# Kernel optimization log

Hardware: AMD Instinct MI355X
Metric: run time of the kernel (lower is better)

Reference implementation:

```python
import jax, jax.numpy as jnp
import numpy as np

B, C, D, H, W = 4, 128, 16, 16, 16
CQ = C // 8

def setup_inputs() -> dict:
    key = jax.random.key(0)
    ks = jax.random.split(key, 8)
    s = 0.05
    return {
        "x": jax.random.normal(ks[0], (B, C, D, H, W), dtype=jnp.float32),
        "wq": jax.random.normal(ks[1], (CQ, C), dtype=jnp.float32) * s,
        "bq": jax.random.normal(ks[2], (CQ,), dtype=jnp.float32) * s,
        "wk": jax.random.normal(ks[3], (CQ, C), dtype=jnp.float32) * s,
        "bk": jax.random.normal(ks[4], (CQ,), dtype=jnp.float32) * s,
        "wv": jax.random.normal(ks[5], (C, C), dtype=jnp.float32) * s,
        "bv": jax.random.normal(ks[6], (C,), dtype=jnp.float32) * s,
        "gamma": jax.random.normal(ks[7], (1,), dtype=jnp.float32),
    }

def reference(x, wq, bq, wk, bk, wv, bv, gamma):
    b, c, d, h, w = x.shape
    n = d * h * w
    xf = x.reshape(b, c, n)                                  # [B,C,N]
    # 1x1x1 convs == channel-wise linear projections
    q = jnp.einsum('bcn,qc->bqn', xf, wq) + bq[None, :, None]  # [B,CQ,N]
    k = jnp.einsum('bcn,qc->bqn', xf, wk) + bk[None, :, None]  # [B,CQ,N]
    v = jnp.einsum('bcn,oc->bon', xf, wv) + bv[None, :, None]  # [B,C,N]
    # energy[b,i,j] = sum_c q[b,c,i] * k[b,c,j]  (query permuted to [B,N,CQ])
    energy = jnp.einsum('bci,bcj->bij', q, k)                # [B,N,N]
    attn = jax.nn.softmax(energy, axis=-1)                   # [B,N,N]
    # out = bmm(value, attn^T): out[b,c,i] = sum_j v[b,c,j] * attn[b,i,j]
    out = jnp.einsum('bcj,bij->bci', v, attn)                # [B,C,N]
    out = out.reshape(b, c, d, h, w)
    return gamma[0] * out + x
```

## Files before the change

### kernel.cpp

```cpp
#include <hip/hip_runtime.h>
#include <stdint.h>

#define NT 4096
#define L2E 1.44269504f

typedef short s16x8 __attribute__((ext_vector_type(8)));
typedef short s16x4 __attribute__((ext_vector_type(4)));
typedef float f32x16 __attribute__((ext_vector_type(16)));
typedef float f32x4 __attribute__((ext_vector_type(4)));
typedef float f32x2 __attribute__((ext_vector_type(2)));

__device__ __forceinline__ unsigned short f2bf(float f) {
  unsigned int u = __float_as_uint(f);
  u = u + 0x7FFFu + ((u >> 16) & 1u);
  return (unsigned short)(u >> 16);
}

__device__ __forceinline__ void pack_pa(const float* p, s16x8* pa) {
  unsigned w8[8];
#pragma unroll
  for (int m = 0; m < 8; ++m)
    asm("v_cvt_pk_bf16_f32 %0, %1, %2" : "=v"(w8[m]) : "v"(p[2 * m]), "v"(p[2 * m + 1]));
  unsigned a0 = w8[0], b0 = w8[2]; asm("v_permlane32_swap_b32 %0, %1" : "+v"(a0), "+v"(b0));
  unsigned a1 = w8[1], b1 = w8[3]; asm("v_permlane32_swap_b32 %0, %1" : "+v"(a1), "+v"(b1));
  unsigned c0 = w8[4], d0 = w8[6]; asm("v_permlane32_swap_b32 %0, %1" : "+v"(c0), "+v"(d0));
  unsigned c1 = w8[5], d1 = w8[7]; asm("v_permlane32_swap_b32 %0, %1" : "+v"(c1), "+v"(d1));
  union PW { unsigned u[4]; s16x8 v; } q0, q1;
  q0.u[0] = a0; q0.u[1] = a1; q0.u[2] = b0; q0.u[3] = b1;
  q1.u[0] = c0; q1.u[1] = c1; q1.u[2] = d0; q1.u[3] = d1;
  pa[0] = q0.v; pa[1] = q1.v;
}

__device__ __forceinline__ void merge_write(float* reg, const f32x16 (&acc)[2][4],
                                            int lc, int hi) {
#pragma unroll
  for (int isub = 0; isub < 2; ++isub)
#pragma unroll
    for (int cb = 0; cb < 4; ++cb)
#pragma unroll
      for (int q = 0; q < 4; ++q) {
        int c0 = 32 * cb + 8 * q + 4 * hi;
        int row = isub * 32 + lc;
        f32x2 a = { acc[isub][cb][q * 4 + 0], acc[isub][cb][q * 4 + 1] };
        f32x2 b2 = { acc[isub][cb][q * 4 + 2], acc[isub][cb][q * 4 + 3] };
        *(f32x2*)(reg + row * 132 + c0) = a;
        *(f32x2*)(reg + row * 132 + c0 + 2) = b2;
      }
}
__device__ __forceinline__ void merge_add(const float* reg, f32x16 (&acc)[2][4],
                                          int lc, int hi) {
#pragma unroll
  for (int isub = 0; isub < 2; ++isub)
#pragma unroll
    for (int cb = 0; cb < 4; ++cb)
#pragma unroll
      for (int q = 0; q < 4; ++q) {
        int c0 = 32 * cb + 8 * q + 4 * hi;
        int row = isub * 32 + lc;
        f32x2 a = *(const f32x2*)(reg + row * 132 + c0);
        f32x2 b2 = *(const f32x2*)(reg + row * 132 + c0 + 2);
        acc[isub][cb][q * 4 + 0] += a[0];
        acc[isub][cb][q * 4 + 1] += a[1];
        acc[isub][cb][q * 4 + 2] += b2[0];
        acc[isub][cb][q * 4 + 3] += b2[1];
      }
}

__global__ __launch_bounds__(512, 2) void proj_kern(
    const float* __restrict__ x,
    const float* __restrict__ wq, const float* __restrict__ bq,
    const float* __restrict__ wk, const float* __restrict__ bk,
    const float* __restrict__ wv, const float* __restrict__ bv,
    short* __restrict__ qws, short* __restrict__ kws, short* __restrict__ vws) {
  __shared__ __align__(16) unsigned short w_s[160 * 128];
  __shared__ __align__(16) unsigned short x_s[128 * 64];

  int t = threadIdx.x;
  int blk = blockIdx.x;
  int b = blk >> 6;
  int n0 = (blk & 63) * 64;

  for (int i4 = t; i4 < 5120; i4 += 512) {
    int row = i4 >> 5, ka = (i4 & 31) * 4;
    f32x4 v;
    float sc = 1.0f;
    if (row < 128)      v = *(const f32x4*)(wv + row * 128 + ka);
    else if (row < 144) v = *(const f32x4*)(wq + (row - 128) * 128 + ka);
    else              { v = *(const f32x4*)(wk + (row - 144) * 128 + ka); sc = L2E; }
    s16x4 o;
#pragma unroll
    for (int j = 0; j < 4; ++j) o[j] = (short)f2bf(v[j] * sc);
    unsigned byt = ((unsigned)(ka * 2)) ^ (((unsigned)row & 7u) << 4);
    *(s16x4*)((char*)w_s + row * 256 + byt) = o;
  }
  {
    int cL = t >> 4, nn4 = (t & 15) * 4;
    for (int cc = 0; cc < 128; cc += 32) {
      int c = cc + cL;
      f32x4 v = *(const f32x4*)(x + ((size_t)b * 128 + c) * NT + n0 + nn4);
      s16x4 o;
#pragma unroll
      for (int j = 0; j < 4; ++j) o[j] = (short)f2bf(v[j]);
      *(s16x4*)(x_s + c * 64 + nn4) = o;
    }
  }
  __syncthreads();

  int w = t >> 6, lane = t & 63, lc = lane & 31, hi = lane >> 5;
  int rblk = w >> 1, nc = w & 1;
  int nn = nc * 32 + lc;

  f32x16 zf = {0.f,0.f,0.f,0.f,0.f,0.f,0.f,0.f,0.f,0.f,0.f,0.f,0.f,0.f,0.f,0.f};
  f32x16 acc = zf, acc2 = zf;

#pragma unroll
  for (int kk = 0; kk < 8; ++kk) {
    int kb0 = kk * 16 + hi * 8;
    s16x8 xf;
#pragma unroll
    for (int e = 0; e < 8; ++e) xf[e] = (short)x_s[(kb0 + e) * 64 + nn];
    unsigned byt = ((unsigned)(kk * 32 + hi * 16)) ^ (((unsigned)lc & 7u) << 4);
    s16x8 af = *(const s16x8*)((const char*)w_s + (rblk * 32 + lc) * 256 + byt);
    acc = __builtin_amdgcn_mfma_f32_32x32x16_bf16(af, xf, acc, 0, 0, 0);
    if (rblk == 3) {
      s16x8 af2 = *(const s16x8*)((const char*)w_s + (128 + lc) * 256 + byt);
      acc2 = __builtin_amdgcn_mfma_f32_32x32x16_bf16(af2, xf, acc2, 0, 0, 0);
    }
  }

#pragma unroll
  for (int r = 0; r < 16; ++r) {
    int c = rblk * 32 + (r & 3) + 8 * (r >> 2) + 4 * hi;
    vws[((size_t)b * 128 + c) * NT + n0 + nn] = (short)f2bf(acc[r] + bv[c]);
  }
  if (rblk == 3) {
    size_t nidx = ((size_t)b * NT + n0 + nn) * 16;
    s16x4 q0, q1, k0, k1;
#pragma unroll
    for (int j = 0; j < 4; ++j) {
      q0[j] = (short)f2bf(acc2[j]      + bq[j + 4 * hi]);
      q1[j] = (short)f2bf(acc2[j + 4]  + bq[j + 8 + 4 * hi]);
      k0[j] = (short)f2bf(acc2[j + 8]  + bk[j + 4 * hi] * L2E);
      k1[j] = (short)f2bf(acc2[j + 12] + bk[j + 8 + 4 * hi] * L2E);
    }
    *(s16x4*)(qws + nidx + 4 * hi)     = q0;
    *(s16x4*)(qws + nidx + 8 + 4 * hi) = q1;
    *(s16x4*)(kws + nidx + 4 * hi)     = k0;
    *(s16x4*)(kws + nidx + 8 + 4 * hi) = k1;
  }
}

__global__ __launch_bounds__(512, 2) void attn_mfma(
    const short* __restrict__ qws, const short* __restrict__ kws, const short* __restrict__ vws,
    const float* __restrict__ x, const float* __restrict__ gp, float* __restrict__ out) {
  __shared__ __align__(16) unsigned char lds[69888];

  int g = blockIdx.x;
  int gg = (g & 7) * 32 + (g >> 3);
  int b = gg >> 6;
  int it = gg & 63;
  int t = threadIdx.x;
  int w = t >> 6, lane = t & 63, lc = lane & 31, hi = lane >> 5;
  int jt0 = w * 512;

  const short* qb = qws + (size_t)b * NT * 16;
  const short* kb = kws + (size_t)b * NT * 16;
  const short* vb = vws + (size_t)b * 128 * NT;

  s16x8 qf0 = *(const s16x8*)(qb + (size_t)(it * 64 + lc) * 16 + hi * 8);
  s16x8 qf1 = *(const s16x8*)(qb + (size_t)(it * 64 + 32 + lc) * 16 + hi * 8);

  unsigned char* tile = lds + w * 8192;
  int ro = lane >> 2, gsl = lane & 3;
  const short* vsrc = vb + (size_t)ro * NT + gsl * 8 + jt0;
  int woff = ro * 64 + ((gsl ^ (ro & 3)) << 4);

  s16x8 stg[8];
#pragma unroll
  for (int rr = 0; rr < 8; ++rr)
    stg[rr] = *(const s16x8*)(vsrc + (size_t)rr * 16 * NT);
#pragma unroll
  for (int rr = 0; rr < 8; ++rr)
    *(s16x8*)(tile + rr * 1024 + woff) = stg[rr];
  s16x8 kf = *(const s16x8*)(kb + (size_t)(jt0 + lc) * 16 + hi * 8);

  f32x16 zf = {0.f,0.f,0.f,0.f,0.f,0.f,0.f,0.f,0.f,0.f,0.f,0.f,0.f,0.f,0.f,0.f};
  f32x16 acc[2][4];
#pragma unroll
  for (int i = 0; i < 2; ++i)
#pragma unroll
    for (int j = 0; j < 4; ++j) acc[i][j] = zf;
  float lsum0 = 0.f, lsum1 = 0.f;

  for (int st = 0; st < 16; ++st) {
    s16x8 kn = kf;
    if (st < 15) {
      const short* vp = vsrc + (st + 1) * 32;
#pragma unroll
      for (int rr = 0; rr < 8; ++rr)
        stg[rr] = *(const s16x8*)(vp + (size_t)rr * 16 * NT);
      kn = *(const s16x8*)(kb + (size_t)(jt0 + (st + 1) * 32 + lc) * 16 + hi * 8);
    }

    f32x16 e0 = __builtin_amdgcn_mfma_f32_32x32x16_bf16(kf, qf0, zf, 0, 0, 0);
    f32x16 e1 = __builtin_amdgcn_mfma_f32_32x32x16_bf16(kf, qf1, zf, 0, 0, 0);

    float p0[16], p1[16];
#pragma unroll
    for (int r = 0; r < 16; ++r) { p0[r] = __builtin_amdgcn_exp2f(e0[r]); p1[r] = __builtin_amdgcn_exp2f(e1[r]); }
    float a0 = 0.f, a1 = 0.f;
#pragma unroll
    for (int r = 0; r < 16; ++r) { a0 += p0[r]; a1 += p1[r]; }
    lsum0 += a0; lsum1 += a1;

    s16x8 pa0[2], pa1[2];
    pack_pa(p0, pa0);
    pack_pa(p1, pa1);

#pragma unroll
    for (int sl = 0; sl < 2; ++sl) {
      int gx = 2 * sl + hi;
#pragma unroll
      for (int cb = 0; cb < 4; ++cb) {
        s16x8 vf = *(const s16x8*)(tile + (cb * 32 + lc) * 64 + ((gx ^ (lc & 3)) << 4));
        acc[0][cb] = __builtin_amdgcn_mfma_f32_32x32x16_bf16(vf, pa0[sl], acc[0][cb], 0, 0, 0);
        acc[1][cb] = __builtin_amdgcn_mfma_f32_32x32x16_bf16(vf, pa1[sl], acc[1][cb], 0, 0, 0);
      }
    }

    if (st < 15) {
#pragma unroll
      for (int rr = 0; rr < 8; ++rr)
        *(s16x8*)(tile + rr * 1024 + woff) = stg[rr];
    }
    kf = kn;
  }

  float* rg0  = (float*)lds;
  float* rg1  = (float*)(lds + 33792);
  float* lsc  = (float*)(lds + 67584);
  float* linv = (float*)(lds + 69632);

  float lf0 = lsum0 + __shfl_xor(lsum0, 32);
  float lf1 = lsum1 + __shfl_xor(lsum1, 32);
  if (hi == 0) { lsc[w * 64 + lc] = lf0; lsc[w * 64 + 32 + lc] = lf1; }
  __syncthreads();
  if (t < 64) {
    float L = 0.f;
#pragma unroll
    for (int w2 = 0; w2 < 8; ++w2) L += lsc[w2 * 64 + t];
    linv[t] = 1.0f / L;
  }
  if (w == 4) merge_write(rg0, acc, lc, hi);
  if (w == 5) merge_write(rg1, acc, lc, hi);
  __syncthreads();
  if (w == 0) merge_add(rg0, acc, lc, hi);
  if (w == 1) merge_add(rg1, acc, lc, hi);
  __syncthreads();
  if (w == 6) merge_write(rg0, acc, lc, hi);
  if (w == 7) merge_write(rg1, acc, lc, hi);
  __syncthreads();
  if (w == 2) merge_add(rg0, acc, lc, hi);
  if (w == 3) merge_add(rg1, acc, lc, hi);
  __syncthreads();
  if (w == 2) merge_write(rg0, acc, lc, hi);
  if (w == 3) merge_write(rg1, acc, lc, hi);
  __syncthreads();
  if (w == 0) merge_add(rg0, acc, lc, hi);
  if (w == 1) merge_add(rg1, acc, lc, hi);
  __syncthreads();
  if (w == 1) merge_write(rg0, acc, lc, hi);
  __syncthreads();
  if (w == 0) {
    merge_add(rg0, acc, lc, hi);
    float li0 = linv[lc], li1 = linv[32 + lc];
#pragma unroll
    for (int cb = 0; cb < 4; ++cb)
#pragma unroll
      for (int r = 0; r < 16; ++r) { acc[0][cb][r] *= li0; acc[1][cb][r] *= li1; }
    merge_write(rg0, acc, lc, hi);
  }
  __syncthreads();

  float gam = gp[0];
  int cc = t >> 2, iq = t & 3;
  const float* xb = x + ((size_t)b * 128 + cc) * NT + it * 64 + iq * 16;
  float* ob = out + ((size_t)b * 128 + cc) * NT + it * 64 + iq * 16;
#pragma unroll
  for (int q2 = 0; q2 < 4; ++q2) {
    f32x4 xv = *(const f32x4*)(xb + q2 * 4);
    f32x4 ov;
#pragma unroll
    for (int j = 0; j < 4; ++j) {
      int i = iq * 16 + q2 * 4 + j;
      ov[j] = gam * rg0[i * 132 + cc] + xv[j];
    }
    *(f32x4*)(ob + q2 * 4) = ov;
  }
}

extern "C" void kernel_launch(void* const* d_in, const int* in_sizes, int n_in,
                              void* d_out, int out_size, void* d_ws, size_t ws_size,
                              hipStream_t stream) {
  const float* x     = (const float*)d_in[0];
  const float* wq    = (const float*)d_in[1];
  const float* bq    = (const float*)d_in[2];
  const float* wk    = (const float*)d_in[3];
  const float* bk    = (const float*)d_in[4];
  const float* wv    = (const float*)d_in[5];
  const float* bv    = (const float*)d_in[6];
  const float* gamma = (const float*)d_in[7];
  float* out = (float*)d_out;

  short* qws = (short*)d_ws;
  short* kws = qws + (size_t)4 * NT * 16;
  short* vws = kws + (size_t)4 * NT * 16;

  proj_kern<<<256, 512, 0, stream>>>(x, wq, bq, wk, bk, wv, bv, qws, kws, vws);
  attn_mfma<<<256, 512, 0, stream>>>(qws, kws, vws, x, gamma, out);
}
```

Measured before the change: 43.79 us.

## Store V in MFMA fragment layout and load it directly, dropping LDS staging

The projection kernel now writes V through an LDS transpose into a fragment-friendly layout, grouped in 16-column blocks of [128 channels x 16 positions]. The attention kernel can then load V operands straight from global memory into registers, with no per-wave LDS tile staging or rewrite. This removes the LDS round trip and swaps the MFMA operand order, which changes the accumulator layout, so the merge helpers are rewritten to match. The softmax normalization moves into the final epilogue. The cost is more global and L2 traffic for V per step, with loads issued in the same iteration they are used and no prefetch.

```diff
diff --git a/kernel.cpp b/kernel.cpp
--- a/kernel.cpp
+++ b/kernel.cpp
@@ -8,7 +8,6 @@
 typedef short s16x4 __attribute__((ext_vector_type(4)));
 typedef float f32x16 __attribute__((ext_vector_type(16)));
 typedef float f32x4 __attribute__((ext_vector_type(4)));
-typedef float f32x2 __attribute__((ext_vector_type(2)));
 
 __device__ __forceinline__ unsigned short f2bf(float f) {
   unsigned int u = __float_as_uint(f);
@@ -31,38 +30,28 @@
   pa[0] = q0.v; pa[1] = q1.v;
 }
 
-__device__ __forceinline__ void merge_write(float* reg, const f32x16 (&acc)[2][4],
+__device__ __forceinline__ void merge_write(float* scr, const f32x16 (&acc)[2][4],
                                             int lc, int hi) {
 #pragma unroll
   for (int isub = 0; isub < 2; ++isub)
 #pragma unroll
     for (int cb = 0; cb < 4; ++cb)
 #pragma unroll
-      for (int q = 0; q < 4; ++q) {
-        int c0 = 32 * cb + 8 * q + 4 * hi;
-        int row = isub * 32 + lc;
-        f32x2 a = { acc[isub][cb][q * 4 + 0], acc[isub][cb][q * 4 + 1] };
-        f32x2 b2 = { acc[isub][cb][q * 4 + 2], acc[isub][cb][q * 4 + 3] };
-        *(f32x2*)(reg + row * 132 + c0) = a;
-        *(f32x2*)(reg + row * 132 + c0 + 2) = b2;
+      for (int r = 0; r < 16; ++r) {
+        int i = isub * 32 + (r & 3) + 8 * (r >> 2) + 4 * hi;
+        scr[i * 132 + cb * 32 + lc] = acc[isub][cb][r];
       }
 }
-__device__ __forceinline__ void merge_add(const float* reg, f32x16 (&acc)[2][4],
+__device__ __forceinline__ void merge_add(const float* scr, f32x16 (&acc)[2][4],
                                           int lc, int hi) {
 #pragma unroll
   for (int isub = 0; isub < 2; ++isub)
 #pragma unroll
     for (int cb = 0; cb < 4; ++cb)
 #pragma unroll
-      for (int q = 0; q < 4; ++q) {
-        int c0 = 32 * cb + 8 * q + 4 * hi;
-        int row = isub * 32 + lc;
-        f32x2 a = *(const f32x2*)(reg + row * 132 + c0);
-        f32x2 b2 = *(const f32x2*)(reg + row * 132 + c0 + 2);
-        acc[isub][cb][q * 4 + 0] += a[0];
-        acc[isub][cb][q * 4 + 1] += a[1];
-        acc[isub][cb][q * 4 + 2] += b2[0];
-        acc[isub][cb][q * 4 + 3] += b2[1];
+      for (int r = 0; r < 16; ++r) {
+        int i = isub * 32 + (r & 3) + 8 * (r >> 2) + 4 * hi;
+        acc[isub][cb][r] += scr[i * 132 + cb * 32 + lc];
       }
 }
 
@@ -71,9 +60,9 @@
     const float* __restrict__ wq, const float* __restrict__ bq,
     const float* __restrict__ wk, const float* __restrict__ bk,
     const float* __restrict__ wv, const float* __restrict__ bv,
-    short* __restrict__ qws, short* __restrict__ kws, short* __restrict__ vws) {
+    short* __restrict__ qws, short* __restrict__ kws, short* __restrict__ vfrag) {
   __shared__ __align__(16) unsigned short w_s[160 * 128];
-  __shared__ __align__(16) unsigned short x_s[128 * 64];
+  __shared__ __align__(16) unsigned short xv_s[128 * 72];
 
   int t = threadIdx.x;
   int blk = blockIdx.x;
@@ -101,7 +90,7 @@
       s16x4 o;
 #pragma unroll
       for (int j = 0; j < 4; ++j) o[j] = (short)f2bf(v[j]);
-      *(s16x4*)(x_s + c * 64 + nn4) = o;
+      *(s16x4*)(xv_s + c * 64 + nn4) = o;
     }
   }
   __syncthreads();
@@ -118,7 +107,7 @@
     int kb0 = kk * 16 + hi * 8;
     s16x8 xf;
 #pragma unroll
-    for (int e = 0; e < 8; ++e) xf[e] = (short)x_s[(kb0 + e) * 64 + nn];
+    for (int e = 0; e < 8; ++e) xf[e] = (short)xv_s[(kb0 + e) * 64 + nn];
     unsigned byt = ((unsigned)(kk * 32 + hi * 16)) ^ (((unsigned)lc & 7u) << 4);
     s16x8 af = *(const s16x8*)((const char*)w_s + (rblk * 32 + lc) * 256 + byt);
     acc = __builtin_amdgcn_mfma_f32_32x32x16_bf16(af, xf, acc, 0, 0, 0);
@@ -128,11 +117,6 @@
     }
   }
 
-#pragma unroll
-  for (int r = 0; r < 16; ++r) {
-    int c = rblk * 32 + (r & 3) + 8 * (r >> 2) + 4 * hi;
-    vws[((size_t)b * 128 + c) * NT + n0 + nn] = (short)f2bf(acc[r] + bv[c]);
-  }
   if (rblk == 3) {
     size_t nidx = ((size_t)b * NT + n0 + nn) * 16;
     s16x4 q0, q1, k0, k1;
@@ -148,10 +132,26 @@
     *(s16x4*)(kws + nidx + 4 * hi)     = k0;
     *(s16x4*)(kws + nidx + 8 + 4 * hi) = k1;
   }
+
+  __syncthreads();
+#pragma unroll
+  for (int r = 0; r < 16; ++r) {
+    int c = rblk * 32 + (r & 3) + 8 * (r >> 2) + 4 * hi;
+    xv_s[c * 72 + nn] = f2bf(acc[r] + bv[c]);
+  }
+  __syncthreads();
+#pragma unroll
+  for (int p = 0; p < 2; ++p) {
+    int gid = t + p * 512;
+    int c = gid & 127, ng = gid >> 7;
+    s16x8 v = *(const s16x8*)(xv_s + c * 72 + ng * 8);
+    size_t idx = (((size_t)b * 256 + (n0 >> 4) + (ng >> 1)) * 128 + c) * 16 + (ng & 1) * 8;
+    *(s16x8*)(vfrag + idx) = v;
+  }
 }
 
 __global__ __launch_bounds__(512, 2) void attn_mfma(
-    const short* __restrict__ qws, const short* __restrict__ kws, const short* __restrict__ vws,
+    const short* __restrict__ qws, const short* __restrict__ kws, const short* __restrict__ vfrag,
     const float* __restrict__ x, const float* __restrict__ gp, float* __restrict__ out) {
   __shared__ __align__(16) unsigned char lds[69888];
 
@@ -165,25 +165,11 @@
 
   const short* qb = qws + (size_t)b * NT * 16;
   const short* kb = kws + (size_t)b * NT * 16;
-  const short* vb = vws + (size_t)b * 128 * NT;
+  const short* vfb = vfrag + (size_t)b * 256 * 128 * 16;
 
   s16x8 qf0 = *(const s16x8*)(qb + (size_t)(it * 64 + lc) * 16 + hi * 8);
   s16x8 qf1 = *(const s16x8*)(qb + (size_t)(it * 64 + 32 + lc) * 16 + hi * 8);
 
-  unsigned char* tile = lds + w * 8192;
-  int ro = lane >> 2, gsl = lane & 3;
-  const short* vsrc = vb + (size_t)ro * NT + gsl * 8 + jt0;
-  int woff = ro * 64 + ((gsl ^ (ro & 3)) << 4);
-
-  s16x8 stg[8];
-#pragma unroll
-  for (int rr = 0; rr < 8; ++rr)
-    stg[rr] = *(const s16x8*)(vsrc + (size_t)rr * 16 * NT);
-#pragma unroll
-  for (int rr = 0; rr < 8; ++rr)
-    *(s16x8*)(tile + rr * 1024 + woff) = stg[rr];
-  s16x8 kf = *(const s16x8*)(kb + (size_t)(jt0 + lc) * 16 + hi * 8);
-
   f32x16 zf = {0.f,0.f,0.f,0.f,0.f,0.f,0.f,0.f,0.f,0.f,0.f,0.f,0.f,0.f,0.f,0.f};
   f32x16 acc[2][4];
 #pragma unroll
@@ -192,15 +178,19 @@
     for (int j = 0; j < 4; ++j) acc[i][j] = zf;
   float lsum0 = 0.f, lsum1 = 0.f;
 
+  s16x8 kf = *(const s16x8*)(kb + (size_t)(jt0 + lc) * 16 + hi * 8);
+
   for (int st = 0; st < 16; ++st) {
+    int jtb = (jt0 >> 4) + st * 2;
+    s16x8 vB[2][4];
+#pragma unroll
+    for (int sl = 0; sl < 2; ++sl)
+#pragma unroll
+      for (int cb = 0; cb < 4; ++cb)
+        vB[sl][cb] = *(const s16x8*)(vfb + ((size_t)(jtb + sl) * 128 + cb * 32 + lc) * 16 + hi * 8);
     s16x8 kn = kf;
-    if (st < 15) {
-      const short* vp = vsrc + (st + 1) * 32;
-#pragma unroll
-      for (int rr = 0; rr < 8; ++rr)
-        stg[rr] = *(const s16x8*)(vp + (size_t)rr * 16 * NT);
+    if (st < 15)
       kn = *(const s16x8*)(kb + (size_t)(jt0 + (st + 1) * 32 + lc) * 16 + hi * 8);
-    }
 
     f32x16 e0 = __builtin_amdgcn_mfma_f32_32x32x16_bf16(kf, qf0, zf, 0, 0, 0);
     f32x16 e1 = __builtin_amdgcn_mfma_f32_32x32x16_bf16(kf, qf1, zf, 0, 0, 0);
@@ -218,21 +208,12 @@
     pack_pa(p1, pa1);
 
 #pragma unroll
-    for (int sl = 0; sl < 2; ++sl) {
-      int gx = 2 * sl + hi;
+    for (int sl = 0; sl < 2; ++sl)
 #pragma unroll
       for (int cb = 0; cb < 4; ++cb) {
-        s16x8 vf = *(const s16x8*)(tile + (cb * 32 + lc) * 64 + ((gx ^ (lc & 3)) << 4));
-        acc[0][cb] = __builtin_amdgcn_mfma_f32_32x32x16_bf16(vf, pa0[sl], acc[0][cb], 0, 0, 0);
-        acc[1][cb] = __builtin_amdgcn_mfma_f32_32x32x16_bf16(vf, pa1[sl], acc[1][cb], 0, 0, 0);
+        acc[0][cb] = __builtin_amdgcn_mfma_f32_32x32x16_bf16(pa0[sl], vB[sl][cb], acc[0][cb], 0, 0, 0);
+        acc[1][cb] = __builtin_amdgcn_mfma_f32_32x32x16_bf16(pa1[sl], vB[sl][cb], acc[1][cb], 0, 0, 0);
       }
-    }
-
-    if (st < 15) {
-#pragma unroll
-      for (int rr = 0; rr < 8; ++rr)
-        *(s16x8*)(tile + rr * 1024 + woff) = stg[rr];
-    }
     kf = kn;
   }
 
@@ -273,11 +254,6 @@
   __syncthreads();
   if (w == 0) {
     merge_add(rg0, acc, lc, hi);
-    float li0 = linv[lc], li1 = linv[32 + lc];
-#pragma unroll
-    for (int cb = 0; cb < 4; ++cb)
-#pragma unroll
-      for (int r = 0; r < 16; ++r) { acc[0][cb][r] *= li0; acc[1][cb][r] *= li1; }
     merge_write(rg0, acc, lc, hi);
   }
   __syncthreads();
@@ -293,7 +269,7 @@
 #pragma unroll
     for (int j = 0; j < 4; ++j) {
       int i = iq * 16 + q2 * 4 + j;
-      ov[j] = gam * rg0[i * 132 + cc] + xv[j];
+      ov[j] = gam * rg0[i * 132 + cc] * linv[i] + xv[j];
     }
     *(f32x4*)(ob + q2 * 4) = ov;
   }
@@ -312,10 +288,10 @@
   const float* gamma = (const float*)d_in[7];
   float* out = (float*)d_out;
 
-  short* qws = (short*)d_ws;
-  short* kws = qws + (size_t)4 * NT * 16;
-  short* vws = kws + (size_t)4 * NT * 16;
-
-  proj_kern<<<256, 512, 0, stream>>>(x, wq, bq, wk, bk, wv, bv, qws, kws, vws);
-  attn_mfma<<<256, 512, 0, stream>>>(qws, kws, vws, x, gamma, out);
-}
+  short* qws   = (short*)d_ws;
+  short* kws   = qws + (size_t)4 * NT * 16;
+  short* vfrag = kws + (size_t)4 * NT * 16;
+
+  proj_kern<<<256, 512, 0, stream>>>(x, wq, bq, wk, bk, wv, bv, qws, kws, vfrag);
+  attn_mfma<<<256, 512, 0, stream>>>(qws, kws, vfrag, x, gamma, out);
+}
```

Result: no change. 43.54 us (-0.6%).
